# Kernel optimization log

Hardware: AMD Instinct MI355X
Metric: run time of the kernel (lower is better)

Reference implementation:

```python
import jax, jax.numpy as jnp
import numpy as np

ENC_H, DEC_H, ATTN = 1024, 1024, 512
B, S = 32, 4096


def setup_inputs() -> dict:
    key = jax.random.key(0)
    k1, k2, k3, k4, k5, k6 = jax.random.split(key, 6)
    decoder_state = jax.random.normal(k1, (B, DEC_H), dtype=jnp.float32)
    encoder_outputs = jax.random.normal(k2, (B, S, ENC_H), dtype=jnp.float32)
    mask = jax.random.randint(k3, (B, S), 0, 2, dtype=jnp.int32)
    W_h = jax.random.normal(k4, (ENC_H, ATTN), dtype=jnp.float32) / np.sqrt(ENC_H)
    W_s = jax.random.normal(k5, (DEC_H, ATTN), dtype=jnp.float32) / np.sqrt(DEC_H)
    v = jax.random.normal(k6, (ATTN,), dtype=jnp.float32) / np.sqrt(ATTN)
    return {"decoder_state": decoder_state, "encoder_outputs": encoder_outputs,
            "mask": mask, "W_h": W_h, "W_s": W_s, "v": v}


def reference(decoder_state, encoder_outputs, mask, W_h, W_s, v):
    # proj_enc: (B, S, A), proj_dec: (B, 1, A)
    proj_enc = jnp.einsum('bse,ea->bsa', encoder_outputs, W_h)
    proj_dec = jnp.einsum('bd,da->ba', decoder_state, W_s)[:, None, :]
    # scores: (B, S) = v^T tanh(W_h h_j + W_s s_i)
    scores = jnp.einsum('bsa,a->bs', jnp.tanh(proj_enc + proj_dec), v)
    neg_inf = jnp.finfo(scores.dtype).min
    scores = jnp.where(mask == 0, neg_inf, scores)
    weights = jax.nn.softmax(scores, axis=-1)  # (B, S)
    context = jnp.einsum('bs,bse->be', weights, encoder_outputs)  # (B, ENC_H)
    return context, weights
```

## Files before the change

### kernel.cpp

```cpp
#include <hip/hip_runtime.h>
#include <hip/hip_bf16.h>
#include <float.h>
#include <math.h>

#define NB 32
#define NS 4096
#define NE 1024
#define ND 1024
#define NA 512

typedef __attribute__((ext_vector_type(4))) float f32x4;
typedef __attribute__((ext_vector_type(8))) short short8;

static __device__ __forceinline__ ushort f2bf(float f){
    union { float f; unsigned int u; } x; x.f = f;
    unsigned int u = x.u + 0x7fffu + ((x.u >> 16) & 1u);
    return (ushort)(u >> 16);
}

static __device__ __forceinline__ float tanh_fast(float x){
    float e = __expf(2.f * x);
    return 1.f - 2.f / (e + 1.f);
}

__global__ __launch_bounds__(256) void k_prep_wtf(const float* __restrict__ Wh,
                                                  ushort* __restrict__ WTf){
    int i = blockIdx.x * 256 + threadIdx.x;
    int e = i & 7;
    int lane = (i >> 3) & 63;
    int ng = (i >> 9) & 31;
    int s = i >> 14;
    int k = s * 32 + (lane >> 4) * 8 + e;
    int col = ng * 16 + (lane & 15);
    WTf[i] = f2bf(Wh[k * NA + col]);
}

__global__ __launch_bounds__(512) void k_projdec(const float* __restrict__ dec,
                                                 const float* __restrict__ Ws,
                                                 float* __restrict__ pdp){
    int b = blockIdx.x >> 2, kc = blockIdx.x & 3;
    int a = threadIdx.x;
    const float* dp = dec + b * ND + kc * 256;
    const float* wp = Ws + (size_t)(kc * 256) * NA + a;
    float acc = 0.f;
    #pragma unroll 4
    for (int k = 0; k < 256; k++) acc += dp[k] * wp[(size_t)k * NA];
    pdp[(kc * NB + b) * NA + a] = acc;
}

__global__ __launch_bounds__(512, 4) void k_scores(const float* __restrict__ E,
                                                   const ushort* __restrict__ WTf,
                                                   const float* __restrict__ pdp,
                                                   const float* __restrict__ v,
                                                   float* __restrict__ scrp){
    const int t = threadIdx.x;
    const int lane = t & 63, w = t >> 6;
    const int l15 = lane & 15, grp = lane >> 4;
    const int wm = w >> 2, wn = w & 3;

    const int bid = blockIdx.x;
    const int xcd = bid & 7, slot = bid >> 3;
    const int mblk = xcd * 128 + (slot >> 1);
    const int bn = slot & 1;
    const int m0 = mblk << 7;
    const int b = mblk >> 5;

    __shared__ __align__(16) ushort bft[2][128 * 64];
    __shared__ float sc[128][4];

    const int sr = t >> 2, sq = t & 3;
    const float* gsrc = E + (size_t)(m0 + sr) * NE + sq * 16;
    const unsigned wb0 = (unsigned)(sr * 128 + ((sq * 32) ^ ((sr & 7) << 4)));

    f32x4 acc[4][4];
    f32x4 zero; zero[0]=0.f; zero[1]=0.f; zero[2]=0.f; zero[3]=0.f;
    #pragma unroll
    for (int m = 0; m < 4; m++)
        #pragma unroll
        for (int n = 0; n < 4; n++) acc[m][n] = zero;

    f32x4 st[4];
    auto stage_load = [&](int it){
        const f32x4* p = (const f32x4*)(gsrc + it * 64);
        st[0] = p[0]; st[1] = p[1]; st[2] = p[2]; st[3] = p[3];
    };
    auto stage_write = [&](int buf){
        short8 h0, h1;
        #pragma unroll
        for (int e = 0; e < 4; e++){
            h0[e]     = (short)__builtin_bit_cast(ushort, __float2bfloat16(st[0][e]));
            h0[e + 4] = (short)__builtin_bit_cast(ushort, __float2bfloat16(st[1][e]));
            h1[e]     = (short)__builtin_bit_cast(ushort, __float2bfloat16(st[2][e]));
            h1[e + 4] = (short)__builtin_bit_cast(ushort, __float2bfloat16(st[3][e]));
        }
        char* base = (char*)&bft[buf][0];
        *(short8*)(base + wb0)        = h0;
        *(short8*)(base + (wb0 ^ 16)) = h1;
    };

    const ushort* wtf0 = WTf + ((size_t)(bn * 16 + wn * 4) * 64 + lane) * 8;

    auto compute_kk = [&](int buf, int kk, short8 (&wt)[4]){
        const char* base = (const char*)&bft[buf][0];
        #pragma unroll
        for (int m = 0; m < 4; m++){
            const int row = wm * 64 + m * 16 + l15;
            short8 af = *(const short8*)(base + row * 128 + (((kk * 4 + grp) * 16) ^ ((row & 7) << 4)));
            #pragma unroll
            for (int n = 0; n < 4; n++)
                acc[m][n] = __builtin_amdgcn_mfma_f32_16x16x32_bf16(af, wt[n], acc[m][n], 0, 0, 0);
        }
    };

    stage_load(0);
    stage_write(0);
    asm volatile("s_waitcnt lgkmcnt(0)" ::: "memory");
    __builtin_amdgcn_s_barrier();

    for (int it = 0; it < 16; ++it){
        const int buf = it & 1;
        short8 wt0[4], wt1[4];
        const ushort* wp0 = wtf0 + (size_t)(it * 2) * 16384;
        #pragma unroll
        for (int n = 0; n < 4; n++) wt0[n] = *(const short8*)(wp0 + n * 512);
        #pragma unroll
        for (int n = 0; n < 4; n++) wt1[n] = *(const short8*)(wp0 + 16384 + n * 512);
        __builtin_amdgcn_sched_barrier(0);
        if (it < 15) stage_load(it + 1);
        __builtin_amdgcn_sched_barrier(0);
        compute_kk(buf, 0, wt0);
        compute_kk(buf, 1, wt1);
        __builtin_amdgcn_sched_barrier(0);
        if (it < 15) stage_write(buf ^ 1);
        asm volatile("s_waitcnt lgkmcnt(0)" ::: "memory");
        __builtin_amdgcn_s_barrier();
    }

    float pdc[4], vc[4];
    #pragma unroll
    for (int n = 0; n < 4; n++){
        int c = bn * 256 + wn * 64 + n * 16 + l15;
        float p = 0.f;
        #pragma unroll
        for (int kc = 0; kc < 4; kc++) p += pdp[(kc * NB + b) * NA + c];
        pdc[n] = p;
        vc[n] = v[c];
    }
    #pragma unroll
    for (int m = 0; m < 4; m++){
        #pragma unroll
        for (int j = 0; j < 4; j++){
            float s = 0.f;
            #pragma unroll
            for (int n = 0; n < 4; n++) s += tanh_fast(acc[m][n][j] + pdc[n]) * vc[n];
            s += __shfl_xor(s, 1);
            s += __shfl_xor(s, 2);
            s += __shfl_xor(s, 4);
            s += __shfl_xor(s, 8);
            if (l15 == 0) sc[wm * 64 + m * 16 + grp * 4 + j][wn] = s;
        }
    }
    __syncthreads();
    if (t < 128)
        scrp[(size_t)bn * (NB * NS) + m0 + t] = sc[t][0] + sc[t][1] + sc[t][2] + sc[t][3];
}

__global__ __launch_bounds__(256) void k_softmax(const float* __restrict__ scrp,
                                                 const int* __restrict__ mask,
                                                 float* __restrict__ weights){
    int b = blockIdx.x, t = threadIdx.x;
    __shared__ float red[8];
    float vals[16];
    float mx = -FLT_MAX;
    #pragma unroll
    for (int i = 0; i < 16; i++){
        int s = i * 256 + t;
        float x = scrp[b * NS + s] + scrp[(size_t)(NB * NS) + b * NS + s];
        x = (mask[b * NS + s] != 0) ? x : -FLT_MAX;
        vals[i] = x;
        mx = fmaxf(mx, x);
    }
    #pragma unroll
    for (int off = 32; off; off >>= 1) mx = fmaxf(mx, __shfl_xor(mx, off));
    int wv = t >> 6;
    if ((t & 63) == 0) red[wv] = mx;
    __syncthreads();
    mx = fmaxf(fmaxf(red[0], red[1]), fmaxf(red[2], red[3]));
    float sum = 0.f;
    #pragma unroll
    for (int i = 0; i < 16; i++){ vals[i] = __expf(vals[i] - mx); sum += vals[i]; }
    #pragma unroll
    for (int off = 32; off; off >>= 1) sum += __shfl_xor(sum, off);
    if ((t & 63) == 0) red[4 + wv] = sum;
    __syncthreads();
    sum = red[4] + red[5] + red[6] + red[7];
    float inv = 1.f / sum;
    #pragma unroll
    for (int i = 0; i < 16; i++) weights[b * NS + i * 256 + t] = vals[i] * inv;
}

__global__ __launch_bounds__(1024) void k_context(const float* __restrict__ E,
                                                  const float* __restrict__ weights,
                                                  float* __restrict__ part){
    int b = blockIdx.x >> 3, ch = blockIdx.x & 7;
    int t = threadIdx.x;
    int h = t >> 8, tg = t & 255;
    __shared__ float wsm[512];
    __shared__ __align__(16) f32x4 red[4][256];
    if (t < 512) wsm[t] = weights[b * NS + ch * 512 + t];
    __syncthreads();
    const f32x4* Ep = (const f32x4*)(E + ((size_t)b * NS + ch * 512 + h * 128) * NE) + tg;
    f32x4 acc; acc[0]=0.f; acc[1]=0.f; acc[2]=0.f; acc[3]=0.f;
    #pragma unroll 4
    for (int s = 0; s < 128; s++){
        f32x4 e = Ep[(size_t)s * 256];
        float w = wsm[h * 128 + s];
        acc[0] += w * e[0]; acc[1] += w * e[1];
        acc[2] += w * e[2]; acc[3] += w * e[3];
    }
    red[h][tg] = acc;
    __syncthreads();
    if (h == 0){
        f32x4 a0 = red[0][tg], a1 = red[1][tg], a2 = red[2][tg], a3 = red[3][tg];
        f32x4 s;
        s[0] = a0[0]+a1[0]+a2[0]+a3[0];
        s[1] = a0[1]+a1[1]+a2[1]+a3[1];
        s[2] = a0[2]+a1[2]+a2[2]+a3[2];
        s[3] = a0[3]+a1[3]+a2[3]+a3[3];
        *(f32x4*)(part + ((size_t)(b * 8 + ch)) * NE + tg * 4) = s;
    }
}

__global__ __launch_bounds__(256) void k_reduce_ctx(const float* __restrict__ part,
                                                    float* __restrict__ ctx){
    int i = blockIdx.x * 256 + threadIdx.x;
    int b = i >> 10, e = i & 1023;
    float s = 0.f;
    #pragma unroll
    for (int ch = 0; ch < 8; ch++) s += part[((size_t)(b * 8 + ch)) * NE + e];
    ctx[i] = s;
}

extern "C" void kernel_launch(void* const* d_in, const int* in_sizes, int n_in,
                              void* d_out, int out_size, void* d_ws, size_t ws_size,
                              hipStream_t stream){
    const float* dec  = (const float*)d_in[0];
    const float* E    = (const float*)d_in[1];
    const int*   mask = (const int*)d_in[2];
    const float* Wh   = (const float*)d_in[3];
    const float* Ws   = (const float*)d_in[4];
    const float* v    = (const float*)d_in[5];
    float* ctx = (float*)d_out;
    float* weights = (float*)d_out + NB * NE;

    char* ws = (char*)d_ws;
    ushort* WTf  = (ushort*)ws;
    float*  part = (float*)ws;
    float*  pdp  = (float*)(ws + (1 << 20));
    float*  scrp = (float*)(ws + (1 << 20) + (256 << 10));

    k_prep_wtf<<<2048, 256, 0, stream>>>(Wh, WTf);
    k_projdec<<<128, 512, 0, stream>>>(dec, Ws, pdp);
    k_scores<<<2048, 512, 0, stream>>>(E, WTf, pdp, v, scrp);
    k_softmax<<<32, 256, 0, stream>>>(scrp, mask, weights);
    k_context<<<256, 1024, 0, stream>>>(E, weights, part);
    k_reduce_ctx<<<128, 256, 0, stream>>>(part, ctx);
}
```

Before: 384.5 us.

## Double score-kernel M tile to 256 rows with interleaved barriered MFMA phases

The scores GEMM block now covers 256 rows of encoder outputs instead of 128, so each wave holds 8x4 accumulators and each bf16 weight fragment loaded from global is reused across twice as many rows. Launch bounds and grid size are halved to match. The K loop is split into four sub-phases, each with barriers and s_setprio around the MFMA bursts, so that waves interleave LDS reads with matrix math. The costs are higher register and LDS use, lower occupancy, and extra barriers per iteration.

```diff
diff --git a/kernel.cpp b/kernel.cpp
--- a/kernel.cpp
+++ b/kernel.cpp
@@ -48,7 +48,7 @@
     pdp[(kc * NB + b) * NA + a] = acc;
 }
 
-__global__ __launch_bounds__(512, 4) void k_scores(const float* __restrict__ E,
+__global__ __launch_bounds__(512, 2) void k_scores(const float* __restrict__ E,
                                                    const ushort* __restrict__ WTf,
                                                    const float* __restrict__ pdp,
                                                    const float* __restrict__ v,
@@ -60,57 +60,46 @@
 
     const int bid = blockIdx.x;
     const int xcd = bid & 7, slot = bid >> 3;
-    const int mblk = xcd * 128 + (slot >> 1);
+    const int mblk = xcd * 64 + (slot >> 1);
     const int bn = slot & 1;
-    const int m0 = mblk << 7;
-    const int b = mblk >> 5;
-
-    __shared__ __align__(16) ushort bft[2][128 * 64];
-    __shared__ float sc[128][4];
-
-    const int sr = t >> 2, sq = t & 3;
-    const float* gsrc = E + (size_t)(m0 + sr) * NE + sq * 16;
-    const unsigned wb0 = (unsigned)(sr * 128 + ((sq * 32) ^ ((sr & 7) << 4)));
-
-    f32x4 acc[4][4];
+    const int m0 = mblk << 8;
+    const int b = mblk >> 4;
+
+    __shared__ __align__(16) ushort bft[2][256 * 64];
+    __shared__ float sc[256][4];
+
+    const int sr = t >> 1, half = t & 1;
+    const float* gsrc = E + (size_t)(m0 + sr) * NE + half * 32;
+
+    f32x4 acc[8][4];
     f32x4 zero; zero[0]=0.f; zero[1]=0.f; zero[2]=0.f; zero[3]=0.f;
     #pragma unroll
-    for (int m = 0; m < 4; m++)
+    for (int m = 0; m < 8; m++)
         #pragma unroll
         for (int n = 0; n < 4; n++) acc[m][n] = zero;
 
-    f32x4 st[4];
+    f32x4 st[8];
     auto stage_load = [&](int it){
         const f32x4* p = (const f32x4*)(gsrc + it * 64);
-        st[0] = p[0]; st[1] = p[1]; st[2] = p[2]; st[3] = p[3];
+        st[0]=p[0]; st[1]=p[1]; st[2]=p[2]; st[3]=p[3];
+        st[4]=p[4]; st[5]=p[5]; st[6]=p[6]; st[7]=p[7];
     };
     auto stage_write = [&](int buf){
-        short8 h0, h1;
-        #pragma unroll
-        for (int e = 0; e < 4; e++){
-            h0[e]     = (short)__builtin_bit_cast(ushort, __float2bfloat16(st[0][e]));
-            h0[e + 4] = (short)__builtin_bit_cast(ushort, __float2bfloat16(st[1][e]));
-            h1[e]     = (short)__builtin_bit_cast(ushort, __float2bfloat16(st[2][e]));
-            h1[e + 4] = (short)__builtin_bit_cast(ushort, __float2bfloat16(st[3][e]));
-        }
-        char* base = (char*)&bft[buf][0];
-        *(short8*)(base + wb0)        = h0;
-        *(short8*)(base + (wb0 ^ 16)) = h1;
-    };
-
-    const ushort* wtf0 = WTf + ((size_t)(bn * 16 + wn * 4) * 64 + lane) * 8;
-
-    auto compute_kk = [&](int buf, int kk, short8 (&wt)[4]){
-        const char* base = (const char*)&bft[buf][0];
-        #pragma unroll
-        for (int m = 0; m < 4; m++){
-            const int row = wm * 64 + m * 16 + l15;
-            short8 af = *(const short8*)(base + row * 128 + (((kk * 4 + grp) * 16) ^ ((row & 7) << 4)));
+        char* bb = (char*)&bft[buf][0];
+        #pragma unroll
+        for (int q = 0; q < 4; ++q){
+            short8 h;
             #pragma unroll
-            for (int n = 0; n < 4; n++)
-                acc[m][n] = __builtin_amdgcn_mfma_f32_16x16x32_bf16(af, wt[n], acc[m][n], 0, 0, 0);
+            for (int e = 0; e < 4; e++){
+                h[e]     = (short)__builtin_bit_cast(ushort, __float2bfloat16(st[2*q][e]));
+                h[e + 4] = (short)__builtin_bit_cast(ushort, __float2bfloat16(st[2*q+1][e]));
+            }
+            unsigned g = (unsigned)(half * 4 + q);
+            *(short8*)(bb + sr * 128 + ((g ^ (unsigned)(sr & 7)) << 4)) = h;
         }
     };
+
+    const ushort* wtf0 = WTf + ((size_t)(bn * 16 + wn * 4) * 64 + lane) * 8;
 
     stage_load(0);
     stage_write(0);
@@ -119,6 +108,8 @@
 
     for (int it = 0; it < 16; ++it){
         const int buf = it & 1;
+        const char* base = (const char*)&bft[buf][0];
+
         short8 wt0[4], wt1[4];
         const ushort* wp0 = wtf0 + (size_t)(it * 2) * 16384;
         #pragma unroll
@@ -128,12 +119,33 @@
         __builtin_amdgcn_sched_barrier(0);
         if (it < 15) stage_load(it + 1);
         __builtin_amdgcn_sched_barrier(0);
-        compute_kk(buf, 0, wt0);
-        compute_kk(buf, 1, wt1);
-        __builtin_amdgcn_sched_barrier(0);
-        if (it < 15) stage_write(buf ^ 1);
-        asm volatile("s_waitcnt lgkmcnt(0)" ::: "memory");
-        __builtin_amdgcn_s_barrier();
+
+        #pragma unroll
+        for (int p = 0; p < 4; ++p){
+            short8 a0k0, a0k1, a1k0, a1k1;
+            {
+                const int r0 = wm * 128 + (2*p)     * 16 + l15;
+                const int r1 = wm * 128 + (2*p + 1) * 16 + l15;
+                a0k0 = *(const short8*)(base + r0 * 128 + (((0u * 4 + grp) ^ (unsigned)(r0 & 7)) << 4));
+                a0k1 = *(const short8*)(base + r0 * 128 + (((1u * 4 + grp) ^ (unsigned)(r0 & 7)) << 4));
+                a1k0 = *(const short8*)(base + r1 * 128 + (((0u * 4 + grp) ^ (unsigned)(r1 & 7)) << 4));
+                a1k1 = *(const short8*)(base + r1 * 128 + (((1u * 4 + grp) ^ (unsigned)(r1 & 7)) << 4));
+            }
+            __builtin_amdgcn_s_barrier();
+            __builtin_amdgcn_s_setprio(1);
+            #pragma unroll
+            for (int n = 0; n < 4; n++){
+                acc[2*p  ][n] = __builtin_amdgcn_mfma_f32_16x16x32_bf16(a0k0, wt0[n], acc[2*p  ][n], 0, 0, 0);
+                acc[2*p  ][n] = __builtin_amdgcn_mfma_f32_16x16x32_bf16(a0k1, wt1[n], acc[2*p  ][n], 0, 0, 0);
+                acc[2*p+1][n] = __builtin_amdgcn_mfma_f32_16x16x32_bf16(a1k0, wt0[n], acc[2*p+1][n], 0, 0, 0);
+                acc[2*p+1][n] = __builtin_amdgcn_mfma_f32_16x16x32_bf16(a1k1, wt1[n], acc[2*p+1][n], 0, 0, 0);
+            }
+            __builtin_amdgcn_s_setprio(0);
+            if (p == 3 && it < 15) stage_write(buf ^ 1);
+            asm volatile("s_waitcnt lgkmcnt(0)" ::: "memory");
+            __builtin_amdgcn_sched_barrier(0);
+            __builtin_amdgcn_s_barrier();
+        }
     }
 
     float pdc[4], vc[4];
@@ -147,7 +159,7 @@
         vc[n] = v[c];
     }
     #pragma unroll
-    for (int m = 0; m < 4; m++){
+    for (int m = 0; m < 8; m++){
         #pragma unroll
         for (int j = 0; j < 4; j++){
             float s = 0.f;
@@ -157,11 +169,11 @@
             s += __shfl_xor(s, 2);
             s += __shfl_xor(s, 4);
             s += __shfl_xor(s, 8);
-            if (l15 == 0) sc[wm * 64 + m * 16 + grp * 4 + j][wn] = s;
+            if (l15 == 0) sc[wm * 128 + m * 16 + grp * 4 + j][wn] = s;
         }
     }
     __syncthreads();
-    if (t < 128)
+    if (t < 256)
         scrp[(size_t)bn * (NB * NS) + m0 + t] = sc[t][0] + sc[t][1] + sc[t][2] + sc[t][3];
 }
 
@@ -261,7 +273,7 @@
 
     k_prep_wtf<<<2048, 256, 0, stream>>>(Wh, WTf);
     k_projdec<<<128, 512, 0, stream>>>(dec, Ws, pdp);
-    k_scores<<<2048, 512, 0, stream>>>(E, WTf, pdp, v, scrp);
+    k_scores<<<1024, 512, 0, stream>>>(E, WTf, pdp, v, scrp);
     k_softmax<<<32, 256, 0, stream>>>(scrp, mask, weights);
     k_context<<<256, 1024, 0, stream>>>(E, weights, part);
     k_reduce_ctx<<<128, 256, 0, stream>>>(part, ctx);
```

Result: slower. 466.4 us (+21.3%).
